# Optimization experiments

Hardware: AMD Instinct MI355X
Metric: run time of the kernel (lower is better)

Reference implementation:

```python
import jax, jax.numpy as jnp
import numpy as np

TOP_K = 2
NUM_EXPERTS = 8

def setup_inputs() -> dict:
    key = jax.random.key(0)
    k_x, k_r, k_g, k_u, k_d = jax.random.split(key, 5)
    B, L, D, H, E = 1, 2048, 1024, 2048, NUM_EXPERTS
    scale = 0.02  # keep router logits / activations in a sane range
    return {
        "x": jax.random.normal(k_x, (B, L, D), dtype=jnp.float32),
        "router_w": jax.random.normal(k_r, (D, E), dtype=jnp.float32) * scale,
        "gate_w": jax.random.normal(k_g, (E, D, H), dtype=jnp.float32) * scale,
        "up_w": jax.random.normal(k_u, (E, D, H), dtype=jnp.float32) * scale,
        "down_w": jax.random.normal(k_d, (E, H, D), dtype=jnp.float32) * scale,
    }

def reference(x, router_w, gate_w, up_w, down_w):
    # x: (B, L, D)
    B, L, D = x.shape
    T = B * L
    E = router_w.shape[1]
    xf = x.reshape(T, D)

    # --- router: top-k softmax over selected logits (Mixtral-style) ---
    logits = xf @ router_w                      # (T, E)
    top_vals, top_idx = jax.lax.top_k(logits, TOP_K)  # (T, K)
    top_w = jax.nn.softmax(top_vals, axis=-1)   # (T, K)

    # combine weights scattered to dense (T, E); zeros for unrouted experts
    combine = jnp.zeros((T, E), dtype=x.dtype).at[
        jnp.arange(T)[:, None], top_idx
    ].add(top_w)

    # --- experts: SwiGLU, computed per expert, zero-weight tokens masked by combine ---
    gate = jnp.einsum('td,edh->eth', xf, gate_w)   # (E, T, H)
    up = jnp.einsum('td,edh->eth', xf, up_w)       # (E, T, H)
    hidden = jax.nn.silu(gate) * up                # (E, T, H)
    expert_out = jnp.einsum('eth,ehd->etd', hidden, down_w)  # (E, T, D)

    # --- weighted combine (equivalent to scatter_add over sorted assignments) ---
    y = jnp.einsum('etd,te->td', expert_out, combine)  # (T, D)
    return y.reshape(B, L, D)
```

## Files before the change

### kernel.cpp

```cpp
#include <hip/hip_runtime.h>
#include <hip/hip_bf16.h>
#include <stdint.h>

#define T_TOK 2048
#define DIM   1024
#define HDIM  2048
#define NE    8
#define ROWS_PAD 4224

typedef __attribute__((ext_vector_type(8))) short bf16x8;
typedef __attribute__((ext_vector_type(4))) float f32x4;

__device__ __forceinline__ unsigned short f2bf(float f) {
    union { float f; unsigned int u; } v; v.f = f;
    unsigned int r = v.u + 0x7FFF + ((v.u >> 16) & 1);
    return (unsigned short)(r >> 16);
}

__device__ __forceinline__ void gload16(const void* g, void* l) {
    __builtin_amdgcn_global_load_lds(
        (const __attribute__((address_space(1))) void*)g,
        (__attribute__((address_space(3))) void*)l, 16, 0, 0);
}

__global__ void transpose_cvt(const float* __restrict__ in, unsigned short* __restrict__ out,
                              int R, int C) {
    __shared__ float tile[32][33];
    int b = blockIdx.z;
    int bx = blockIdx.x, by = blockIdx.y;
    int tx = threadIdx.x & 31, ty = threadIdx.x >> 5;
    const float* ip = in + (size_t)b * R * C;
    unsigned short* op = out + (size_t)b * R * C;
#pragma unroll
    for (int i = 0; i < 4; ++i) {
        int r = by * 32 + ty + i * 8;
        tile[ty + i * 8][tx] = ip[(size_t)r * C + bx * 32 + tx];
    }
    __syncthreads();
#pragma unroll
    for (int i = 0; i < 4; ++i) {
        int oc = bx * 32 + ty + i * 8;
        int orw = by * 32 + tx;
        op[(size_t)oc * R + orw] = f2bf(tile[tx][ty + i * 8]);
    }
}

__global__ void router_kernel(const float* __restrict__ x, const float* __restrict__ rw,
                              int* __restrict__ counts, int* __restrict__ top_idx,
                              float* __restrict__ top_w) {
    int wid = (blockIdx.x * blockDim.x + threadIdx.x) >> 6;
    int lane = threadIdx.x & 63;
    if (wid >= T_TOK) return;
    float acc[NE];
#pragma unroll
    for (int e = 0; e < NE; ++e) acc[e] = 0.f;
    const float* xr = x + (size_t)wid * DIM;
    for (int i = lane; i < DIM; i += 64) {
        float xv = xr[i];
        const float* wr = rw + (size_t)i * NE;
#pragma unroll
        for (int e = 0; e < NE; ++e) acc[e] += xv * wr[e];
    }
#pragma unroll
    for (int off = 32; off; off >>= 1) {
#pragma unroll
        for (int e = 0; e < NE; ++e) acc[e] += __shfl_xor(acc[e], off, 64);
    }
    if (lane == 0) {
        float v0 = -1e30f, v1 = -1e30f; int i0 = 0, i1 = 0;
#pragma unroll
        for (int e = 0; e < NE; ++e) {
            float v = acc[e];
            if (v > v0) { v1 = v0; i1 = i0; v0 = v; i0 = e; }
            else if (v > v1) { v1 = v; i1 = e; }
        }
        float e1 = __expf(v1 - v0);
        float s = 1.f + e1;
        top_idx[wid * 2]     = i0;
        top_idx[wid * 2 + 1] = i1;
        top_w[wid * 2]     = 1.f / s;
        top_w[wid * 2 + 1] = e1 / s;
        atomicAdd(&counts[i0], 1);
        atomicAdd(&counts[i1], 1);
    }
}

__global__ void scan_kernel(const int* __restrict__ counts, int* __restrict__ offsets,
                            int* __restrict__ cursors) {
    if (threadIdx.x == 0) {
        int run = 0;
        for (int e = 0; e < NE; ++e) { offsets[e] = run; cursors[e] = run; run += counts[e]; }
    }
}

__global__ void gather_kernel(const float* __restrict__ x, const int* __restrict__ top_idx,
                              const float* __restrict__ top_w, int* __restrict__ cursors,
                              int* __restrict__ row_tok, float* __restrict__ row_w,
                              unsigned short* __restrict__ Abuf) {
    int t = blockIdx.x;
    __shared__ int pos[2];
    if (threadIdx.x < 2) {
        int k = threadIdx.x;
        int e = top_idx[t * 2 + k];
        int p = atomicAdd(&cursors[e], 1);
        pos[k] = p;
        row_tok[p] = t;
        row_w[p] = top_w[t * 2 + k];
    }
    __syncthreads();
    const float4* xr = (const float4*)(x + (size_t)t * DIM);
    float4 v = xr[threadIdx.x];
    ushort4 b;
    b.x = f2bf(v.x); b.y = f2bf(v.y); b.z = f2bf(v.z); b.w = f2bf(v.w);
    ushort4* A4 = (ushort4*)Abuf;
    A4[(size_t)pos[0] * (DIM / 4) + threadIdx.x] = b;
    A4[(size_t)pos[1] * (DIM / 4) + threadIdx.x] = b;
}

__global__ __launch_bounds__(256, 2)
void gemm1_kernel(const unsigned short* __restrict__ Abuf,
                  const unsigned short* __restrict__ WgT,
                  const unsigned short* __restrict__ WuT,
                  unsigned short* __restrict__ Hbuf,
                  const int* __restrict__ offsets, const int* __restrict__ counts) {
    const int e = blockIdx.z;
    const int cnt = counts[e];
    const int mtile = blockIdx.y;
    if (mtile * 128 >= cnt) return;
    const int n0 = blockIdx.x * 128;
    const int row0 = offsets[e] + mtile * 128;

    __shared__ unsigned short As[3][128 * 32];
    __shared__ unsigned short Bg[3][128 * 32];
    __shared__ unsigned short Bu[3][128 * 32];

    const int tid = threadIdx.x;
    const int lane = tid & 63;
    const int wave = tid >> 6;
    const int wm = wave >> 1, wn = wave & 1;

    f32x4 accg[4][4], accu[4][4];
#pragma unroll
    for (int i = 0; i < 4; ++i)
#pragma unroll
        for (int j = 0; j < 4; ++j) {
            accg[i][j] = (f32x4){0.f, 0.f, 0.f, 0.f};
            accu[i][j] = (f32x4){0.f, 0.f, 0.f, 0.f};
        }

    const int srow0 = tid >> 2;
    const int sc0 = tid & 3;
    const unsigned short* Aab = Abuf + (size_t)row0 * DIM;
    const unsigned short* Bgb = WgT + (size_t)e * HDIM * DIM + (size_t)n0 * DIM;
    const unsigned short* Bub = WuT + (size_t)e * HDIM * DIM + (size_t)n0 * DIM;

    auto stage = [&](int buf, int kt) {
#pragma unroll
        for (int i = 0; i < 2; ++i) {
            int row = i * 64 + srow0;
            int csrc = sc0 ^ ((row >> 1) & 3);
            size_t go = (size_t)row * DIM + kt + csrc * 8;
            int lo = (i * 256 + tid) * 8;
            gload16(Aab + go, &As[buf][lo]);
            gload16(Bgb + go, &Bg[buf][lo]);
            gload16(Bub + go, &Bu[buf][lo]);
        }
    };

    const int rsel = lane & 15;
    const int csrcf = lane >> 4;

    const int NS = DIM / 32;
    stage(0, 0);
    stage(1, 32);
    int cur = 0;
    for (int s = 0; s < NS; ++s) {
        if (s + 1 < NS) { asm volatile("s_waitcnt vmcnt(6)" ::: "memory"); }
        else            { asm volatile("s_waitcnt vmcnt(0)" ::: "memory"); }
        __builtin_amdgcn_s_barrier();
        if (s + 2 < NS) {
            int pb = cur + 2; if (pb >= 3) pb -= 3;
            stage(pb, (s + 2) * 32);
        }
        const unsigned short* Ac = As[cur];
        const unsigned short* Bgc = Bg[cur];
        const unsigned short* Buc = Bu[cur];
        bf16x8 af[4], bg[4], bu[4];
#pragma unroll
        for (int i = 0; i < 4; ++i) {
            int ra = wm * 64 + i * 16 + rsel;
            af[i] = *(const bf16x8*)&Ac[ra * 32 + (csrcf ^ ((ra >> 1) & 3)) * 8];
            int rb = wn * 64 + i * 16 + rsel;
            int cb = (csrcf ^ ((rb >> 1) & 3)) * 8;
            bg[i] = *(const bf16x8*)&Bgc[rb * 32 + cb];
            bu[i] = *(const bf16x8*)&Buc[rb * 32 + cb];
        }
#pragma unroll
        for (int i = 0; i < 4; ++i)
#pragma unroll
            for (int j = 0; j < 4; ++j) {
                accg[i][j] = __builtin_amdgcn_mfma_f32_16x16x32_bf16(af[i], bg[j], accg[i][j], 0, 0, 0);
                accu[i][j] = __builtin_amdgcn_mfma_f32_16x16x32_bf16(af[i], bu[j], accu[i][j], 0, 0, 0);
            }
        ++cur; if (cur == 3) cur = 0;
    }

    const int c = lane & 15, rbase = (lane >> 4) * 4;
    const int obase = offsets[e];
#pragma unroll
    for (int i = 0; i < 4; ++i) {
#pragma unroll
        for (int r = 0; r < 4; ++r) {
            int lrow = mtile * 128 + wm * 64 + i * 16 + rbase + r;
            if (lrow < cnt) {
                size_t orow = (size_t)(obase + lrow);
#pragma unroll
                for (int j = 0; j < 4; ++j) {
                    float g = accg[i][j][r], u = accu[i][j][r];
                    float h = g * u / (1.f + __expf(-g));
                    Hbuf[orow * HDIM + n0 + wn * 64 + j * 16 + c] = f2bf(h);
                }
            }
        }
    }
}

__global__ __launch_bounds__(256, 3)
void gemm2_kernel(const unsigned short* __restrict__ Hbuf,
                  const unsigned short* __restrict__ WdT,
                  float* __restrict__ y,
                  const int* __restrict__ offsets, const int* __restrict__ counts,
                  const int* __restrict__ row_tok, const float* __restrict__ row_w) {
    const int e = blockIdx.z >> 1;
    const int kc = blockIdx.z & 1;
    const int cnt = counts[e];
    const int mtile = blockIdx.y;
    if (mtile * 128 >= cnt) return;
    const int n0 = blockIdx.x * 128;
    const int row0 = offsets[e] + mtile * 128;

    __shared__ unsigned short As[3][128 * 32];
    __shared__ unsigned short Bs[3][128 * 32];

    const int tid = threadIdx.x;
    const int lane = tid & 63;
    const int wave = tid >> 6;
    const int wm = wave >> 1, wn = wave & 1;

    f32x4 acc[4][4];
#pragma unroll
    for (int i = 0; i < 4; ++i)
#pragma unroll
        for (int j = 0; j < 4; ++j) acc[i][j] = (f32x4){0.f, 0.f, 0.f, 0.f};

    const int srow0 = tid >> 2;
    const int sc0 = tid & 3;
    const unsigned short* Aab = Hbuf + (size_t)row0 * HDIM;
    const unsigned short* Bbb = WdT + (size_t)e * DIM * HDIM + (size_t)n0 * HDIM;

    auto stage = [&](int buf, int kt) {
#pragma unroll
        for (int i = 0; i < 2; ++i) {
            int row = i * 64 + srow0;
            int csrc = sc0 ^ ((row >> 1) & 3);
            size_t go = (size_t)row * HDIM + kt + csrc * 8;
            int lo = (i * 256 + tid) * 8;
            gload16(Aab + go, &As[buf][lo]);
            gload16(Bbb + go, &Bs[buf][lo]);
        }
    };

    const int rsel = lane & 15;
    const int csrcf = lane >> 4;

    const int kbeg = kc * (HDIM / 2);
    const int NS = (HDIM / 2) / 32;

    stage(0, kbeg);
    stage(1, kbeg + 32);
    int cur = 0;
    for (int s = 0; s < NS; ++s) {
        if (s + 1 < NS) { asm volatile("s_waitcnt vmcnt(4)" ::: "memory"); }
        else            { asm volatile("s_waitcnt vmcnt(0)" ::: "memory"); }
        __builtin_amdgcn_s_barrier();
        if (s + 2 < NS) {
            int pb = cur + 2; if (pb >= 3) pb -= 3;
            stage(pb, kbeg + (s + 2) * 32);
        }
        const unsigned short* Ac = As[cur];
        const unsigned short* Bc = Bs[cur];
        bf16x8 af[4], bf[4];
#pragma unroll
        for (int i = 0; i < 4; ++i) {
            int ra = wm * 64 + i * 16 + rsel;
            af[i] = *(const bf16x8*)&Ac[ra * 32 + (csrcf ^ ((ra >> 1) & 3)) * 8];
            int rb = wn * 64 + i * 16 + rsel;
            bf[i] = *(const bf16x8*)&Bc[rb * 32 + (csrcf ^ ((rb >> 1) & 3)) * 8];
        }
#pragma unroll
        for (int i = 0; i < 4; ++i)
#pragma unroll
            for (int j = 0; j < 4; ++j)
                acc[i][j] = __builtin_amdgcn_mfma_f32_16x16x32_bf16(af[i], bf[j], acc[i][j], 0, 0, 0);
        ++cur; if (cur == 3) cur = 0;
    }

    const int c = lane & 15, rbase = (lane >> 4) * 4;
    const int obase = offsets[e];
#pragma unroll
    for (int i = 0; i < 4; ++i) {
#pragma unroll
        for (int r = 0; r < 4; ++r) {
            int lrow = mtile * 128 + wm * 64 + i * 16 + rbase + r;
            if (lrow < cnt) {
                int grow = obase + lrow;
                int tok = row_tok[grow];
                float w = row_w[grow];
#pragma unroll
                for (int j = 0; j < 4; ++j) {
                    atomicAdd(&y[(size_t)tok * DIM + n0 + wn * 64 + j * 16 + c], w * acc[i][j][r]);
                }
            }
        }
    }
}

extern "C" void kernel_launch(void* const* d_in, const int* in_sizes, int n_in,
                              void* d_out, int out_size, void* d_ws, size_t ws_size,
                              hipStream_t stream) {
    const float* x  = (const float*)d_in[0];
    const float* rw = (const float*)d_in[1];
    const float* gw = (const float*)d_in[2];
    const float* uw = (const float*)d_in[3];
    const float* dw = (const float*)d_in[4];
    float* y = (float*)d_out;

    char* ws = (char*)d_ws;
    int*   counts  = (int*)(ws + 0);
    int*   cursors = (int*)(ws + 32);
    int*   offsets = (int*)(ws + 64);
    int*   top_idx = (int*)(ws + 128);
    float* top_w   = (float*)(ws + 128 + 16384);
    int*   row_tok = (int*)(ws + 128 + 32768);
    float* row_w   = (float*)(ws + 128 + 32768 + 16896);
    size_t off = 128 + 32768 + 2 * 16896;
    off = (off + 255) & ~(size_t)255;
    unsigned short* Abuf = (unsigned short*)(ws + off); off += (size_t)ROWS_PAD * DIM * 2;
    unsigned short* Hbuf = (unsigned short*)(ws + off); off += (size_t)ROWS_PAD * HDIM * 2;
    unsigned short* WgT  = (unsigned short*)(ws + off); off += (size_t)NE * DIM * HDIM * 2;
    unsigned short* WuT  = (unsigned short*)(ws + off); off += (size_t)NE * DIM * HDIM * 2;
    unsigned short* WdT  = (unsigned short*)(ws + off); off += (size_t)NE * DIM * HDIM * 2;
    if (ws_size < off) return;

    hipMemsetAsync(counts, 0, 32, stream);
    hipMemsetAsync(d_out, 0, (size_t)out_size * 4, stream);

    transpose_cvt<<<dim3(HDIM / 32, DIM / 32, NE), 256, 0, stream>>>(gw, WgT, DIM, HDIM);
    transpose_cvt<<<dim3(HDIM / 32, DIM / 32, NE), 256, 0, stream>>>(uw, WuT, DIM, HDIM);
    transpose_cvt<<<dim3(DIM / 32, HDIM / 32, NE), 256, 0, stream>>>(dw, WdT, HDIM, DIM);

    router_kernel<<<T_TOK / 4, 256, 0, stream>>>(x, rw, counts, top_idx, top_w);
    scan_kernel<<<1, 64, 0, stream>>>(counts, offsets, cursors);
    gather_kernel<<<T_TOK, 256, 0, stream>>>(x, top_idx, top_w, cursors, row_tok, row_w, Abuf);

    gemm1_kernel<<<dim3(HDIM / 128, 16, NE), 256, 0, stream>>>(Abuf, WgT, WuT, Hbuf, offsets, counts);
    gemm2_kernel<<<dim3(DIM / 128, 16, NE * 2), 256, 0, stream>>>(Hbuf, WdT, y, offsets, counts, row_tok, row_w);
}
```

Before: 285.5 us.

## Compact expert tile list, vectorize transpose stores, simplify gemm1 to double buffering

```diff
diff --git a/kernel.cpp b/kernel.cpp
--- a/kernel.cpp
+++ b/kernel.cpp
@@ -7,6 +7,7 @@
 #define HDIM  2048
 #define NE    8
 #define ROWS_PAD 4224
+#define TSLOTS 40
 
 typedef __attribute__((ext_vector_type(8))) short bf16x8;
 typedef __attribute__((ext_vector_type(4))) float f32x4;
@@ -38,10 +39,13 @@
     }
     __syncthreads();
 #pragma unroll
-    for (int i = 0; i < 4; ++i) {
-        int oc = bx * 32 + ty + i * 8;
-        int orw = by * 32 + tx;
-        op[(size_t)oc * R + orw] = f2bf(tile[tx][ty + i * 8]);
+    for (int i = 0; i < 2; ++i) {
+        int oc = i * 16 + (threadIdx.x >> 4);
+        int orw2 = (threadIdx.x & 15) * 2;
+        ushort2 v;
+        v.x = f2bf(tile[orw2][oc]);
+        v.y = f2bf(tile[orw2 + 1][oc]);
+        *(ushort2*)&op[(size_t)(bx * 32 + oc) * R + by * 32 + orw2] = v;
     }
 }
 
@@ -86,10 +90,17 @@
 }
 
 __global__ void scan_kernel(const int* __restrict__ counts, int* __restrict__ offsets,
-                            int* __restrict__ cursors) {
+                            int* __restrict__ cursors,
+                            int* __restrict__ tl_e, int* __restrict__ tl_m) {
     if (threadIdx.x == 0) {
         int run = 0;
         for (int e = 0; e < NE; ++e) { offsets[e] = run; cursors[e] = run; run += counts[e]; }
+        int n = 0;
+        for (int e = 0; e < NE; ++e) {
+            int mt = (counts[e] + 127) >> 7;
+            for (int m = 0; m < mt && n < 64; ++m) { tl_e[n] = e; tl_m[n] = m; ++n; }
+        }
+        for (; n < 64; ++n) tl_e[n] = -1;
     }
 }
 
@@ -122,17 +133,19 @@
                   const unsigned short* __restrict__ WgT,
                   const unsigned short* __restrict__ WuT,
                   unsigned short* __restrict__ Hbuf,
-                  const int* __restrict__ offsets, const int* __restrict__ counts) {
-    const int e = blockIdx.z;
+                  const int* __restrict__ offsets, const int* __restrict__ counts,
+                  const int* __restrict__ tl_e, const int* __restrict__ tl_m) {
+    const int slot = blockIdx.y;
+    const int e = tl_e[slot];
+    if (e < 0) return;
+    const int mtile = tl_m[slot];
     const int cnt = counts[e];
-    const int mtile = blockIdx.y;
-    if (mtile * 128 >= cnt) return;
     const int n0 = blockIdx.x * 128;
     const int row0 = offsets[e] + mtile * 128;
 
-    __shared__ unsigned short As[3][128 * 32];
-    __shared__ unsigned short Bg[3][128 * 32];
-    __shared__ unsigned short Bu[3][128 * 32];
+    __shared__ unsigned short As[2][128 * 32];
+    __shared__ unsigned short Bg[2][128 * 32];
+    __shared__ unsigned short Bu[2][128 * 32];
 
     const int tid = threadIdx.x;
     const int lane = tid & 63;
@@ -170,18 +183,11 @@
     const int rsel = lane & 15;
     const int csrcf = lane >> 4;
 
-    const int NS = DIM / 32;
     stage(0, 0);
-    stage(1, 32);
     int cur = 0;
-    for (int s = 0; s < NS; ++s) {
-        if (s + 1 < NS) { asm volatile("s_waitcnt vmcnt(6)" ::: "memory"); }
-        else            { asm volatile("s_waitcnt vmcnt(0)" ::: "memory"); }
-        __builtin_amdgcn_s_barrier();
-        if (s + 2 < NS) {
-            int pb = cur + 2; if (pb >= 3) pb -= 3;
-            stage(pb, (s + 2) * 32);
-        }
+    for (int kt = 0; kt < DIM; kt += 32) {
+        __syncthreads();
+        if (kt + 32 < DIM) stage(cur ^ 1, kt + 32);
         const unsigned short* Ac = As[cur];
         const unsigned short* Bgc = Bg[cur];
         const unsigned short* Buc = Bu[cur];
@@ -202,7 +208,7 @@
                 accg[i][j] = __builtin_amdgcn_mfma_f32_16x16x32_bf16(af[i], bg[j], accg[i][j], 0, 0, 0);
                 accu[i][j] = __builtin_amdgcn_mfma_f32_16x16x32_bf16(af[i], bu[j], accu[i][j], 0, 0, 0);
             }
-        ++cur; if (cur == 3) cur = 0;
+        cur ^= 1;
     }
 
     const int c = lane & 15, rbase = (lane >> 4) * 4;
@@ -230,12 +236,14 @@
                   const unsigned short* __restrict__ WdT,
                   float* __restrict__ y,
                   const int* __restrict__ offsets, const int* __restrict__ counts,
-                  const int* __restrict__ row_tok, const float* __restrict__ row_w) {
-    const int e = blockIdx.z >> 1;
-    const int kc = blockIdx.z & 1;
+                  const int* __restrict__ row_tok, const float* __restrict__ row_w,
+                  const int* __restrict__ tl_e, const int* __restrict__ tl_m) {
+    const int slot = blockIdx.y;
+    const int e = tl_e[slot];
+    if (e < 0) return;
+    const int mtile = tl_m[slot];
+    const int kc = blockIdx.z;
     const int cnt = counts[e];
-    const int mtile = blockIdx.y;
-    if (mtile * 128 >= cnt) return;
     const int n0 = blockIdx.x * 128;
     const int row0 = offsets[e] + mtile * 128;
 
@@ -343,7 +351,9 @@
     float* top_w   = (float*)(ws + 128 + 16384);
     int*   row_tok = (int*)(ws + 128 + 32768);
     float* row_w   = (float*)(ws + 128 + 32768 + 16896);
-    size_t off = 128 + 32768 + 2 * 16896;
+    int*   tl_e    = (int*)(ws + 128 + 32768 + 2 * 16896);
+    int*   tl_m    = (int*)(ws + 128 + 32768 + 2 * 16896 + 256);
+    size_t off = 128 + 32768 + 2 * 16896 + 512;
     off = (off + 255) & ~(size_t)255;
     unsigned short* Abuf = (unsigned short*)(ws + off); off += (size_t)ROWS_PAD * DIM * 2;
     unsigned short* Hbuf = (unsigned short*)(ws + off); off += (size_t)ROWS_PAD * HDIM * 2;
@@ -360,9 +370,11 @@
     transpose_cvt<<<dim3(DIM / 32, HDIM / 32, NE), 256, 0, stream>>>(dw, WdT, HDIM, DIM);
 
     router_kernel<<<T_TOK / 4, 256, 0, stream>>>(x, rw, counts, top_idx, top_w);
-    scan_kernel<<<1, 64, 0, stream>>>(counts, offsets, cursors);
+    scan_kernel<<<1, 64, 0, stream>>>(counts, offsets, cursors, tl_e, tl_m);
     gather_kernel<<<T_TOK, 256, 0, stream>>>(x, top_idx, top_w, cursors, row_tok, row_w, Abuf);
 
-    gemm1_kernel<<<dim3(HDIM / 128, 16, NE), 256, 0, stream>>>(Abuf, WgT, WuT, Hbuf, offsets, counts);
-    gemm2_kernel<<<dim3(DIM / 128, 16, NE * 2), 256, 0, stream>>>(Hbuf, WdT, y, offsets, counts, row_tok, row_w);
-}
+    gemm1_kernel<<<dim3(HDIM / 128, TSLOTS), 256, 0, stream>>>(Abuf, WgT, WuT, Hbuf,
+                                                               offsets, counts, tl_e, tl_m);
+    gemm2_kernel<<<dim3(DIM / 128, TSLOTS, 2), 256, 0, stream>>>(Hbuf, WdT, y, offsets, counts,
+                                                                 row_tok, row_w, tl_e, tl_m);
+}
```

Result: faster. 278.8 us (-2.4%).
